# Performance work log

Measured on AMD Instinct MI355X. Metric: run time of the kernel, lower is better.

Reference implementation:

```python
import jax, jax.numpy as jnp
import numpy as np

N = 50000
E = 1600000
B = 64
NODE_DIM = 12
EDGE_DIM = 4
HIDDEN = 128
HEADS = 4
C = HIDDEN // HEADS  # 32
LAYERS = 3
NEG_SLOPE = 0.2
EPS = 1e-16


def _ln(x, g, b):
    m = jnp.mean(x, -1, keepdims=True)
    v = jnp.mean((x - m) ** 2, -1, keepdims=True)
    return (x - m) * jax.lax.rsqrt(v + 1e-5) * g + b


def _gelu(x):
    return jax.nn.gelu(x, approximate=False)


def setup_inputs() -> dict:
    key = jax.random.key(0)
    ks = jax.random.split(key, 20)
    f = lambda k, sh: jax.random.normal(k, sh, jnp.float32) * 0.05
    return {
        "x": jax.random.normal(ks[0], (N, NODE_DIM), jnp.float32),
        "edge_attr": jax.random.normal(ks[1], (E, EDGE_DIM), jnp.float32),
        "edge_index": jax.random.randint(ks[2], (2, E), 0, N, jnp.int32),
        "batch": jnp.sort(jax.random.randint(ks[3], (N,), 0, B, jnp.int32)),
        "enc_w": f(ks[4], (NODE_DIM, HIDDEN)), "enc_b": jnp.zeros(HIDDEN, jnp.float32),
        "enc_g": jnp.ones(HIDDEN, jnp.float32), "enc_beta": jnp.zeros(HIDDEN, jnp.float32),
        "ee_w": f(ks[5], (EDGE_DIM, HIDDEN // 2)), "ee_b": jnp.zeros(HIDDEN // 2, jnp.float32),
        "gat_lin_w": f(ks[6], (LAYERS, HIDDEN, HEADS * C)),
        "gat_edge_w": f(ks[7], (LAYERS, HIDDEN // 2, HEADS * C)),
        "att_src": f(ks[8], (LAYERS, HEADS, C)),
        "att_dst": f(ks[9], (LAYERS, HEADS, C)),
        "att_edge": f(ks[10], (LAYERS, HEADS, C)),
        "gat_bias": jnp.zeros((LAYERS, HEADS * C), jnp.float32),
        "norm_g": jnp.ones((LAYERS, HIDDEN), jnp.float32),
        "norm_b": jnp.zeros((LAYERS, HIDDEN), jnp.float32),
        "freq_w1": f(ks[11], (2 * HIDDEN, HIDDEN)), "freq_b1": jnp.zeros(HIDDEN, jnp.float32),
        "freq_w2": f(ks[12], (HIDDEN, HIDDEN // 2)), "freq_b2": jnp.zeros(HIDDEN // 2, jnp.float32),
        "cls_w1": f(ks[13], (HIDDEN // 2, 64)), "cls_b1": jnp.zeros(64, jnp.float32),
        "cls_w2": f(ks[14], (64, 1)), "cls_b2": jnp.zeros(1, jnp.float32),
    }


def _forward(x, edge_attr, edge_index, batch,
             enc_w, enc_b, enc_g, enc_beta, ee_w, ee_b,
             gat_lin_w, gat_edge_w, att_src, att_dst, att_edge, gat_bias,
             norm_g, norm_b, freq_w1, freq_b1, freq_w2, freq_b2,
             cls_w1, cls_b1, cls_w2, cls_b2):
    n = x.shape[0]
    h = _gelu(_ln(x @ enc_w + enc_b, enc_g, enc_beta))          # [N, HIDDEN]
    ea = _gelu(edge_attr @ ee_w + ee_b)                          # [E, HIDDEN//2]
    src, dst = edge_index[0], edge_index[1]
    # add_self_loops with fill_value='mean': per-dst-node mean of incoming edge attrs
    deg = jax.ops.segment_sum(jnp.ones(src.shape, ea.dtype), dst, n)
    loop_attr = jax.ops.segment_sum(ea, dst, n) / jnp.maximum(deg, 1.0)[:, None]
    ar = jnp.arange(n, dtype=src.dtype)
    s_full = jnp.concatenate([src, ar])
    d_full = jnp.concatenate([dst, ar])
    ea_full = jnp.concatenate([ea, loop_attr], 0)                # [E+N, HIDDEN//2]
    for l in range(LAYERS):
        hh = (h @ gat_lin_w[l]).reshape(n, HEADS, C)             # [N, H, C]
        ef = (ea_full @ gat_edge_w[l]).reshape(-1, HEADS, C)     # [E+N, H, C]
        a_s = jnp.einsum('nhc,hc->nh', hh, att_src[l])
        a_d = jnp.einsum('nhc,hc->nh', hh, att_dst[l])
        alpha = a_s[s_full] + a_d[d_full] + jnp.einsum('ehc,hc->eh', ef, att_edge[l])
        alpha = jnp.where(alpha > 0, alpha, NEG_SLOPE * alpha)   # leaky_relu
        m = jax.ops.segment_max(alpha, d_full, n)                # segment softmax
        ex = jnp.exp(alpha - m[d_full])
        denom = jax.ops.segment_sum(ex, d_full, n)
        w = ex / (denom[d_full] + EPS)                           # [E+N, H]
        agg = jax.ops.segment_sum(w[:, :, None] * hh[s_full], d_full, n)
        agg = agg.reshape(n, HEADS * C) + gat_bias[l]
        h = _ln(h + agg, norm_g[l], norm_b[l])                   # residual + LayerNorm
    cnt = jax.ops.segment_sum(jnp.ones((n,), h.dtype), batch, B)
    mean = jax.ops.segment_sum(h, batch, B) / jnp.maximum(cnt, 1.0)[:, None]
    mx = jax.ops.segment_max(h, batch, B)
    mx = jnp.where(cnt[:, None] > 0, mx, 0.0)
    g = jnp.concatenate([mean, mx], -1)                          # [B, 2*HIDDEN]
    g = _gelu(_gelu(g @ freq_w1 + freq_b1) @ freq_w2 + freq_b2)
    logits = _gelu(g @ cls_w1 + cls_b1) @ cls_w2 + cls_b2
    return jax.nn.sigmoid(logits[:, 0])                          # [B]


def reference(x, edge_attr, edge_index, batch,
              enc_w, enc_b, enc_g, enc_beta, ee_w, ee_b,
              gat_lin_w, gat_edge_w, att_src, att_dst, att_edge, gat_bias,
              norm_g, norm_b, freq_w1, freq_b1, freq_w2, freq_b2,
              cls_w1, cls_b1, cls_w2, cls_b2):
    return _forward(x, edge_attr, edge_index, batch,
                    enc_w, enc_b, enc_g, enc_beta, ee_w, ee_b,
                    gat_lin_w, gat_edge_w, att_src, att_dst, att_edge, gat_bias,
                    norm_g, norm_b, freq_w1, freq_b1, freq_w2, freq_b2,
                    cls_w1, cls_b1, cls_w2, cls_b2)
```

## Files before the change

### kernel.cpp

```cpp
#include <hip/hip_runtime.h>
#include <float.h>
#include <math.h>

#define N_NODES 50000
#define N_EDGES 1600000
#define NB      64
#define HID     128
#define TOT     (N_EDGES + N_NODES)
#define PARTS   16
#define SCAN_NB 196
#define NPART   8
#define PSIZE   6250
#define EPB     1024
#define GM_ROWS 64

typedef __attribute__((ext_vector_type(8))) short short8;
typedef __attribute__((ext_vector_type(4))) float f32x4;
typedef __attribute__((ext_vector_type(2))) float f32x2;

__device__ __forceinline__ float gelu_f(float x){
    return 0.5f * x * (1.0f + erff(x * 0.70710678118654752440f));
}

__device__ __forceinline__ float asf(unsigned int u){
    union { unsigned int i; float f; } c; c.i = u; return c.f;
}
__device__ __forceinline__ float bf2f(unsigned short u){
    return asf(((unsigned int)u) << 16);
}
__device__ __forceinline__ unsigned short f2bf(float x){
    union { float f; unsigned int i; } c; c.f = x;
    unsigned int r = c.i + 0x7fffu + ((c.i >> 16) & 1u);
    return (unsigned short)(r >> 16);
}
__device__ __forceinline__ uint2 pack4(float a, float b, float cc, float d){
    uint2 r;
    r.x = (unsigned int)f2bf(a) | ((unsigned int)f2bf(b) << 16);
    r.y = (unsigned int)f2bf(cc) | ((unsigned int)f2bf(d) << 16);
    return r;
}
__device__ __forceinline__ unsigned short sel_head(uint2 v, int hd){
    return (hd & 2) ? ((hd & 1) ? (unsigned short)(v.y >> 16) : (unsigned short)(v.y & 0xffff))
                    : ((hd & 1) ? (unsigned short)(v.x >> 16) : (unsigned short)(v.x & 0xffff));
}

__device__ __forceinline__ float blk_sum128(float v, float* red){
    #pragma unroll
    for (int m = 32; m > 0; m >>= 1) v += __shfl_xor(v, m, 64);
    __syncthreads();
    if ((threadIdx.x & 63) == 0) red[threadIdx.x >> 6] = v;
    __syncthreads();
    float r = red[0] + red[1];
    __syncthreads();
    return r;
}

__device__ __forceinline__ int blk_scan256(int v, int* wsum){
    int t = threadIdx.x, lane = t & 63, w = t >> 6;
    int x = v;
    #pragma unroll
    for (int off = 1; off < 64; off <<= 1){
        int y = __shfl_up(x, off, 64);
        if (lane >= off) x += y;
    }
    if (lane == 63) wsum[w] = x;
    __syncthreads();
    if (t == 0){
        int s = 0;
        #pragma unroll
        for (int i = 0; i < 4; i++){ int tmp = wsum[i]; wsum[i] = s; s += tmp; }
    }
    __syncthreads();
    return x + wsum[w];
}

__global__ void enc_kernel(const float* __restrict__ x, const float* __restrict__ enc_w,
                           const float* __restrict__ enc_b, const float* __restrict__ enc_g,
                           const float* __restrict__ enc_beta, float* __restrict__ h)
{
    __shared__ float xs[12];
    __shared__ float red[2];
    int n = blockIdx.x, t = threadIdx.x;
    if (t < 12) xs[t] = x[n * 12 + t];
    __syncthreads();
    float acc = enc_b[t];
    #pragma unroll
    for (int k = 0; k < 12; k++) acc += xs[k] * enc_w[k * HID + t];
    float mean = blk_sum128(acc, red) * (1.0f / HID);
    float d = acc - mean;
    float var = blk_sum128(d * d, red) * (1.0f / HID);
    float y = d * rsqrtf(var + 1e-5f) * enc_g[t] + enc_beta[t];
    h[(size_t)n * HID + t] = gelu_f(y);
}

__global__ void count_kernel(const int* __restrict__ ei, int* __restrict__ row_count){
    int part = blockIdx.x & (NPART - 1);
    int slice = blockIdx.x >> 3;
    int lo = part * PSIZE, hi = lo + PSIZE;
    int base = slice * EPB;
    int iend = min(base + EPB, N_EDGES);
    for (int i = base + threadIdx.x; i < iend; i += 256){
        int d = ei[N_EDGES + i];
        if (d >= lo && d < hi) atomicAdd(&row_count[d], 1);
    }
}

__global__ void scan1_kernel(const int* __restrict__ row_count, int* __restrict__ bsum){
    __shared__ int ws[4];
    int i = blockIdx.x * 256 + threadIdx.x;
    int v = (i < N_NODES) ? (row_count[i] + 1) : 0;
    int x = v;
    #pragma unroll
    for (int m = 32; m > 0; m >>= 1) x += __shfl_xor(x, m, 64);
    if ((threadIdx.x & 63) == 0) ws[threadIdx.x >> 6] = x;
    __syncthreads();
    if (threadIdx.x == 0) bsum[blockIdx.x] = ws[0] + ws[1] + ws[2] + ws[3];
}

__global__ void scan2_kernel(int* __restrict__ bsum){
    __shared__ int ws[4];
    int t = threadIdx.x;
    int v = (t < SCAN_NB) ? bsum[t] : 0;
    int incl = blk_scan256(v, ws);
    if (t < SCAN_NB) bsum[t] = incl - v;
}

__global__ void scan3_kernel(const int* __restrict__ row_count, const int* __restrict__ bsum,
                             int* __restrict__ row_ptr, int* __restrict__ cursor){
    __shared__ int ws[4];
    int i = blockIdx.x * 256 + threadIdx.x;
    int v = (i < N_NODES) ? (row_count[i] + 1) : 0;
    int incl = blk_scan256(v, ws) + bsum[blockIdx.x];
    if (i < N_NODES){
        row_ptr[i + 1] = incl;
        cursor[i] = incl - v;
    }
    if (i == 0) row_ptr[0] = 0;
}

__global__ void scatter_kernel(const int* __restrict__ ei, int* __restrict__ cursor,
                               int2* __restrict__ csr_se, int* __restrict__ self_pos,
                               uint2* __restrict__ alp0, uint2* __restrict__ alp1,
                               uint2* __restrict__ alp2){
    int part = blockIdx.x & (NPART - 1);
    int slice = blockIdx.x >> 3;
    int lo = part * PSIZE, hi = lo + PSIZE;
    int base = slice * EPB;
    int iend = min(base + EPB, TOT);
    for (int i = base + threadIdx.x; i < iend; i += 256){
        int d = (i < N_EDGES) ? ei[N_EDGES + i] : (i - N_EDGES);
        if (d < lo || d >= hi) continue;
        int s = (i < N_EDGES) ? ei[i] : d;
        int pos = atomicAdd(&cursor[d], 1);
        csr_se[pos] = make_int2(s, i);
        if (i >= N_EDGES){
            self_pos[d] = pos;
            uint2 z = make_uint2(0u, 0u);
            alp0[pos] = z; alp1[pos] = z; alp2[pos] = z;
        }
    }
}

__global__ void we3_kernel(const float* __restrict__ gat_edge_w, const float* __restrict__ att_edge,
                           float* __restrict__ We3)
{
    int t = threadIdx.x;
    int k = t >> 2, hd = t & 3;
    for (int l = 0; l < 3; l++){
        float s = 0.f;
        #pragma unroll
        for (int c = 0; c < 32; c++)
            s += gat_edge_w[(size_t)l * 64 * HID + k * HID + hd * 32 + c]
               * att_edge[l * HID + hd * 32 + c];
        We3[(l * 64 + k) * 4 + hd] = s;
    }
}

__global__ void ae_pos_kernel(const int2* __restrict__ csr_se, const float4* __restrict__ edge_attr,
                              const float* __restrict__ ee_w, const float* __restrict__ ee_b,
                              const float* __restrict__ We3,
                              uint2* __restrict__ alp0, uint2* __restrict__ alp1,
                              uint2* __restrict__ alp2)
{
    int p = blockIdx.x * 256 + threadIdx.x;
    if (p >= TOT) return;
    int2 se = csr_se[p];
    if (se.y >= N_EDGES) return;
    float4 ea = edge_attr[se.y];
    const f32x2* w0 = (const f32x2*)(ee_w);
    const f32x2* w1 = (const f32x2*)(ee_w + 64);
    const f32x2* w2 = (const f32x2*)(ee_w + 128);
    const f32x2* w3 = (const f32x2*)(ee_w + 192);
    const f32x2* bb = (const f32x2*)(ee_b);
    const f32x2* Wv = (const f32x2*)(We3);

    f32x2 eax = {ea.x, ea.x}, eay = {ea.y, ea.y}, eaz = {ea.z, ea.z}, eaw = {ea.w, ea.w};
    const f32x2 one2 = {1.0f, 1.0f};
    const f32x2 c044 = {0.044715f, 0.044715f};
    const f32x2 kneg = {-2.3021182f, -2.3021182f};

    f32x2 acc[6];
    #pragma unroll
    for (int i = 0; i < 6; i++) acc[i] = (f32x2){0.f, 0.f};

    #pragma unroll 4
    for (int m = 0; m < 32; m++){
        f32x2 u = bb[m];
        u = __builtin_elementwise_fma(eax, w0[m], u);
        u = __builtin_elementwise_fma(eay, w1[m], u);
        u = __builtin_elementwise_fma(eaz, w2[m], u);
        u = __builtin_elementwise_fma(eaw, w3[m], u);
        f32x2 a = u * u;
        f32x2 b = __builtin_elementwise_fma(c044, a, one2);
        f32x2 c = u * kneg;
        f32x2 z = c * b;
        f32x2 e = { exp2f(z.x), exp2f(z.y) };
        f32x2 d = e + one2;
        f32x2 r = { __builtin_amdgcn_rcpf(d.x), __builtin_amdgcn_rcpf(d.y) };
        f32x2 g = u * r;
        f32x2 gx = {g.x, g.x}, gy = {g.y, g.y};
        #pragma unroll
        for (int l = 0; l < 3; l++){
            int base = (l * 64 + 2 * m) * 2;
            acc[l*2+0] = __builtin_elementwise_fma(gx, Wv[base + 0], acc[l*2+0]);
            acc[l*2+1] = __builtin_elementwise_fma(gx, Wv[base + 1], acc[l*2+1]);
            acc[l*2+0] = __builtin_elementwise_fma(gy, Wv[base + 2], acc[l*2+0]);
            acc[l*2+1] = __builtin_elementwise_fma(gy, Wv[base + 3], acc[l*2+1]);
        }
    }
    alp0[p] = pack4(acc[0].x, acc[0].y, acc[1].x, acc[1].y);
    alp1[p] = pack4(acc[2].x, acc[2].y, acc[3].x, acc[3].y);
    alp2[p] = pack4(acc[4].x, acc[4].y, acc[5].x, acc[5].y);
}

__global__ __launch_bounds__(64) void selfae_kernel(
        const int* __restrict__ row_ptr, const int* __restrict__ self_pos,
        uint2* __restrict__ alp0, uint2* __restrict__ alp1, uint2* __restrict__ alp2)
{
    int n = blockIdx.x, t = threadIdx.x;
    int start = row_ptr[n], end = row_ptr[n + 1];
    int sp = self_pos[n];
    float v[12];
    #pragma unroll
    for (int i = 0; i < 12; i++) v[i] = 0.f;
    for (int p = start + t; p < end; p += 64){
        uint2 q0 = alp0[p], q1 = alp1[p], q2 = alp2[p];
        v[0] += asf(q0.x << 16); v[1] += asf(q0.x & 0xffff0000u);
        v[2] += asf(q0.y << 16); v[3] += asf(q0.y & 0xffff0000u);
        v[4] += asf(q1.x << 16); v[5] += asf(q1.x & 0xffff0000u);
        v[6] += asf(q1.y << 16); v[7] += asf(q1.y & 0xffff0000u);
        v[8] += asf(q2.x << 16); v[9] += asf(q2.x & 0xffff0000u);
        v[10] += asf(q2.y << 16); v[11] += asf(q2.y & 0xffff0000u);
    }
    #pragma unroll
    for (int m = 1; m < 64; m <<= 1){
        #pragma unroll
        for (int i = 0; i < 12; i++) v[i] += __shfl_xor(v[i], m, 64);
    }
    if (t == 0){
        float inv = 1.0f / (float)max(end - start - 1, 1);
        alp0[sp] = pack4(v[0]*inv, v[1]*inv, v[2]*inv,  v[3]*inv);
        alp1[sp] = pack4(v[4]*inv, v[5]*inv, v[6]*inv,  v[7]*inv);
        alp2[sp] = pack4(v[8]*inv, v[9]*inv, v[10]*inv, v[11]*inv);
    }
}

__global__ __launch_bounds__(256) void gemm_hh_kernel(
        const float* __restrict__ h, const float* __restrict__ W,
        const float* __restrict__ att_s, const float* __restrict__ att_d,
        unsigned char* __restrict__ hh8, float* __restrict__ a_s,
        float* __restrict__ a_d)
{
    __shared__ __align__(16) unsigned char smem[128 * 136 * 2];
    unsigned short* Wt = (unsigned short*)smem;
    float* Dsh = (float*)smem;
    int t = threadIdx.x;

    for (int i = t; i < 128 * 128; i += 256){
        int k = i >> 7, n = i & 127;
        Wt[n * 136 + k] = f2bf(W[i]);
    }
    __syncthreads();

    int wave = t >> 6, lane = t & 63;
    int mm = lane & 15, quad = lane >> 4;
    int row = blockIdx.x * GM_ROWS + wave * 16 + mm;
    int rclamp = min(row, N_NODES - 1);
    const float* hrow = h + (size_t)rclamp * HID;

    f32x4 acc[8];
    #pragma unroll
    for (int i = 0; i < 8; i++) acc[i] = (f32x4){0.f, 0.f, 0.f, 0.f};

    #pragma unroll
    for (int kc = 0; kc < 4; kc++){
        int k0 = kc * 32 + quad * 8;
        float4 a0 = *(const float4*)(hrow + k0);
        float4 a1 = *(const float4*)(hrow + k0 + 4);
        short8 af;
        af[0] = (short)f2bf(a0.x); af[1] = (short)f2bf(a0.y);
        af[2] = (short)f2bf(a0.z); af[3] = (short)f2bf(a0.w);
        af[4] = (short)f2bf(a1.x); af[5] = (short)f2bf(a1.y);
        af[6] = (short)f2bf(a1.z); af[7] = (short)f2bf(a1.w);
        #pragma unroll
        for (int nt = 0; nt < 8; nt++){
            short8 bf = *(const short8*)&Wt[(nt * 16 + mm) * 136 + k0];
            acc[nt] = __builtin_amdgcn_mfma_f32_16x16x32_bf16(af, bf, acc[nt], 0, 0, 0);
        }
    }
    __syncthreads();

    #pragma unroll
    for (int nt = 0; nt < 8; nt++){
        #pragma unroll
        for (int r = 0; r < 4; r++){
            Dsh[(wave * 16 + quad * 4 + r) * 132 + nt * 16 + mm] = acc[nt][r];
        }
    }
    __syncthreads();

    int c = t & 127, rp = t >> 7;
    float as_w = att_s[c], ad_w = att_d[c];
    int head = c >> 5;
    for (int rr = rp; rr < GM_ROWS; rr += 2){
        int n = blockIdx.x * GM_ROWS + rr;
        if (n >= N_NODES) break;
        float val = Dsh[rr * 132 + c];
        unsigned int pk = (unsigned int)__builtin_amdgcn_cvt_pk_fp8_f32(val, 0.f, 0, false);
        hh8[(size_t)n * HID + c] = (unsigned char)(pk & 0xFFu);
        float vs = val * as_w, vd = val * ad_w;
        #pragma unroll
        for (int m2 = 16; m2 > 0; m2 >>= 1){
            vs += __shfl_xor(vs, m2, 32);
            vd += __shfl_xor(vd, m2, 32);
        }
        if ((c & 31) == 0){
            a_s[n * 4 + head] = vs;
            a_d[n * 4 + head] = vd;
        }
    }
}

__global__ __launch_bounds__(64) void agg_kernel(
        const float* __restrict__ a_s, const float* __restrict__ a_d,
        const int* __restrict__ row_ptr, const int2* __restrict__ csr_se,
        const uint2* __restrict__ alp, const uint2* __restrict__ hhv2,
        float* __restrict__ h, const float* __restrict__ gat_bias,
        const float* __restrict__ norm_g, const float* __restrict__ norm_b)
{
    int n = blockIdx.x, ln = threadIdx.x;
    int g = ln >> 4, l16 = ln & 15, hd = l16 >> 2;
    int start = row_ptr[n], end = row_ptr[n + 1];
    float ad_h = a_d[n * 4 + hd];

    f32x2 a01A = {0.f,0.f}, a23A = {0.f,0.f}, a45A = {0.f,0.f}, a67A = {0.f,0.f};
    f32x2 a01B = {0.f,0.f}, a23B = {0.f,0.f}, a45B = {0.f,0.f}, a67B = {0.f,0.f};
    float exA = 0.f, exB = 0.f;

    auto step = [&](int pp, f32x2& a01, f32x2& a23, f32x2& a45, f32x2& a67, float& es){
        int2 se = csr_se[pp];
        uint2 av = alp[pp];
        float ae = bf2f(sel_head(av, hd));
        float x0 = a_s[se.x * 4 + hd] + ad_h + ae;
        x0 = x0 > 0.f ? x0 : 0.2f * x0;
        float e0 = __expf(x0);
        es += e0;
        uint2 q = hhv2[(size_t)se.x * 16 + l16];
        f32x2 c01 = __builtin_amdgcn_cvt_pk_f32_fp8(q.x, false);
        f32x2 c23 = __builtin_amdgcn_cvt_pk_f32_fp8(q.x, true);
        f32x2 c45 = __builtin_amdgcn_cvt_pk_f32_fp8(q.y, false);
        f32x2 c67 = __builtin_amdgcn_cvt_pk_f32_fp8(q.y, true);
        f32x2 ee = {e0, e0};
        a01 = __builtin_elementwise_fma(ee, c01, a01);
        a23 = __builtin_elementwise_fma(ee, c23, a23);
        a45 = __builtin_elementwise_fma(ee, c45, a45);
        a67 = __builtin_elementwise_fma(ee, c67, a67);
    };

    int p = start + g;
    for (; p + 4 < end; p += 8){
        step(p,     a01A, a23A, a45A, a67A, exA);
        step(p + 4, a01B, a23B, a45B, a67B, exB);
    }
    if (p < end) step(p, a01A, a23A, a45A, a67A, exA);

    f32x2 a01 = a01A + a01B, a23 = a23A + a23B, a45 = a45A + a45B, a67 = a67A + a67B;
    float ex = exA + exB;
    #pragma unroll
    for (int m = 16; m <= 32; m <<= 1){
        a01.x += __shfl_xor(a01.x, m, 64); a01.y += __shfl_xor(a01.y, m, 64);
        a23.x += __shfl_xor(a23.x, m, 64); a23.y += __shfl_xor(a23.y, m, 64);
        a45.x += __shfl_xor(a45.x, m, 64); a45.y += __shfl_xor(a45.y, m, 64);
        a67.x += __shfl_xor(a67.x, m, 64); a67.y += __shfl_xor(a67.y, m, 64);
        ex += __shfl_xor(ex, m, 64);
    }
    float invd = 1.0f / (ex + 1e-16f);

    const float4* hrow4 = (const float4*)(h + (size_t)n * HID);
    float4 hv0 = hrow4[l16 * 2], hv1 = hrow4[l16 * 2 + 1];
    float4 b0 = ((const float4*)gat_bias)[l16 * 2];
    float4 b1 = ((const float4*)gat_bias)[l16 * 2 + 1];
    float y0 = hv0.x + a01.x * invd + b0.x;
    float y1 = hv0.y + a01.y * invd + b0.y;
    float y2 = hv0.z + a23.x * invd + b0.z;
    float y3 = hv0.w + a23.y * invd + b0.w;
    float y4 = hv1.x + a45.x * invd + b1.x;
    float y5 = hv1.y + a45.y * invd + b1.y;
    float y6 = hv1.z + a67.x * invd + b1.z;
    float y7 = hv1.w + a67.y * invd + b1.w;

    float s = y0 + y1 + y2 + y3 + y4 + y5 + y6 + y7;
    #pragma unroll
    for (int m = 1; m <= 8; m <<= 1) s += __shfl_xor(s, m, 64);
    float mean = s * (1.0f / HID);
    float d0 = y0 - mean, d1 = y1 - mean, d2 = y2 - mean, d3 = y3 - mean;
    float d4 = y4 - mean, d5 = y5 - mean, d6 = y6 - mean, d7 = y7 - mean;
    float vsum = d0*d0 + d1*d1 + d2*d2 + d3*d3 + d4*d4 + d5*d5 + d6*d6 + d7*d7;
    #pragma unroll
    for (int m = 1; m <= 8; m <<= 1) vsum += __shfl_xor(vsum, m, 64);
    float rstd = rsqrtf(vsum * (1.0f / HID) + 1e-5f);

    if (ln < 16){
        float4 g0 = ((const float4*)norm_g)[l16 * 2];
        float4 g1 = ((const float4*)norm_g)[l16 * 2 + 1];
        float4 nb0 = ((const float4*)norm_b)[l16 * 2];
        float4 nb1 = ((const float4*)norm_b)[l16 * 2 + 1];
        float4 r0 = make_float4(d0 * rstd * g0.x + nb0.x, d1 * rstd * g0.y + nb0.y,
                                d2 * rstd * g0.z + nb0.z, d3 * rstd * g0.w + nb0.w);
        float4 r1 = make_float4(d4 * rstd * g1.x + nb1.x, d5 * rstd * g1.y + nb1.y,
                                d6 * rstd * g1.z + nb1.z, d7 * rstd * g1.w + nb1.w);
        float4* orow = (float4*)(h + (size_t)n * HID);
        orow[l16 * 2] = r0;
        orow[l16 * 2 + 1] = r1;
    }
}

__global__ void bounds_kernel(const int* __restrict__ batch, int* __restrict__ bstart){
    int b = threadIdx.x;
    if (b > NB) return;
    int lo = 0, hi = N_NODES;
    while (lo < hi){
        int mid = (lo + hi) >> 1;
        if (batch[mid] < b) lo = mid + 1; else hi = mid;
    }
    bstart[b] = lo;
}

__global__ void pool_kernel(const float* __restrict__ h, const int* __restrict__ bstart,
                            float* __restrict__ psum, float* __restrict__ pmax){
    int b = blockIdx.x, part = blockIdx.y, t = threadIdx.x;
    int s = bstart[b], e = bstart[b + 1];
    int len = e - s;
    int chunk = (len + PARTS - 1) / PARTS;
    int cs = s + part * chunk;
    int ce = min(cs + chunk, e);
    float sum = 0.f, mx = -FLT_MAX;
    for (int n = cs; n < ce; ++n){
        float v = h[(size_t)n * HID + t];
        sum += v; mx = fmaxf(mx, v);
    }
    int slot = (b * PARTS + part) * HID + t;
    psum[slot] = sum;
    pmax[slot] = mx;
}

__global__ void mlp_kernel(const float* __restrict__ psum, const float* __restrict__ pmax,
                           const int* __restrict__ bstart,
                           const float* __restrict__ fw1, const float* __restrict__ fb1,
                           const float* __restrict__ fw2, const float* __restrict__ fb2,
                           const float* __restrict__ cw1, const float* __restrict__ cb1,
                           const float* __restrict__ cw2, const float* __restrict__ cb2,
                           float* __restrict__ out)
{
    __shared__ float g[256];
    __shared__ float y1[128];
    __shared__ float y2[64];
    __shared__ float y3[64];
    __shared__ float red[2];
    int b = blockIdx.x, t = threadIdx.x;
    float sum = 0.f, mx = -FLT_MAX;
    for (int p = 0; p < PARTS; p++){
        int slot = (b * PARTS + p) * HID + t;
        sum += psum[slot];
        mx = fmaxf(mx, pmax[slot]);
    }
    int cnt = bstart[b + 1] - bstart[b];
    float mean = sum / (float)max(cnt, 1);
    if (cnt <= 0) mx = 0.f;
    g[t] = mean; g[128 + t] = mx;
    __syncthreads();
    float a1 = fb1[t];
    for (int k = 0; k < 256; k++) a1 += g[k] * fw1[k * 128 + t];
    y1[t] = gelu_f(a1);
    __syncthreads();
    if (t < 64){
        float a2 = fb2[t];
        for (int k = 0; k < 128; k++) a2 += y1[k] * fw2[k * 64 + t];
        y2[t] = gelu_f(a2);
    }
    __syncthreads();
    if (t < 64){
        float a3 = cb1[t];
        for (int k = 0; k < 64; k++) a3 += y2[k] * cw1[k * 64 + t];
        y3[t] = gelu_f(a3);
    }
    __syncthreads();
    float v = (t < 64) ? y3[t] * cw2[t] : 0.f;
    float s = blk_sum128(v, red);
    if (t == 0){
        float logit = s + cb2[0];
        out[b] = 1.0f / (1.0f + expf(-logit));
    }
}

extern "C" void kernel_launch(void* const* d_in, const int* in_sizes, int n_in,
                              void* d_out, int out_size, void* d_ws, size_t ws_size,
                              hipStream_t stream)
{
    const float* x         = (const float*)d_in[0];
    const float* edge_attr = (const float*)d_in[1];
    const int*   edge_idx  = (const int*)  d_in[2];
    const int*   batch     = (const int*)  d_in[3];
    const float* enc_w     = (const float*)d_in[4];
    const float* enc_b     = (const float*)d_in[5];
    const float* enc_g     = (const float*)d_in[6];
    const float* enc_beta  = (const float*)d_in[7];
    const float* ee_w      = (const float*)d_in[8];
    const float* ee_b      = (const float*)d_in[9];
    const float* gat_lin_w = (const float*)d_in[10];
    const float* gat_edge_w= (const float*)d_in[11];
    const float* att_src   = (const float*)d_in[12];
    const float* att_dst   = (const float*)d_in[13];
    const float* att_edge  = (const float*)d_in[14];
    const float* gat_bias  = (const float*)d_in[15];
    const float* norm_g    = (const float*)d_in[16];
    const float* norm_b    = (const float*)d_in[17];
    const float* fw1       = (const float*)d_in[18];
    const float* fb1       = (const float*)d_in[19];
    const float* fw2       = (const float*)d_in[20];
    const float* fb2       = (const float*)d_in[21];
    const float* cw1       = (const float*)d_in[22];
    const float* cb1       = (const float*)d_in[23];
    const float* cw2       = (const float*)d_in[24];
    const float* cb2       = (const float*)d_in[25];
    float* out = (float*)d_out;

    char* wsp = (char*)d_ws;
    size_t off = 0;
    auto alloc = [&](size_t bytes) -> void* {
        void* p = wsp + off;
        off += (bytes + 255) & ~(size_t)255;
        return p;
    };
    float*          h        = (float*)alloc((size_t)N_NODES * HID * 4);
    unsigned char*  hh8      = (unsigned char*)alloc((size_t)N_NODES * HID);
    float*          a_s      = (float*)alloc((size_t)N_NODES * 4 * 4);
    float*          a_d      = (float*)alloc((size_t)N_NODES * 4 * 4);
    uint2*          alp0     = (uint2*)alloc((size_t)TOT * 8);
    uint2*          alp1     = (uint2*)alloc((size_t)TOT * 8);
    uint2*          alp2     = (uint2*)alloc((size_t)TOT * 8);
    int2*           csr_se   = (int2*) alloc((size_t)TOT * 8);
    int*            self_pos = (int*)  alloc((size_t)N_NODES * 4);
    int*            row_ptr  = (int*)  alloc((size_t)(N_NODES + 1) * 4);
    int*            cursor   = (int*)  alloc((size_t)N_NODES * 4);
    int*            row_count= (int*)  alloc((size_t)N_NODES * 4);
    int*            bsum     = (int*)  alloc((size_t)SCAN_NB * 4);
    float*          We3      = (float*)alloc(3 * 64 * 4 * 4);
    int*            bstart   = (int*)  alloc((NB + 1) * 4);
    float*          psum     = (float*)alloc((size_t)NB * PARTS * HID * 4);
    float*          pmax     = (float*)alloc((size_t)NB * PARTS * HID * 4);

    hipLaunchKernelGGL(enc_kernel, dim3(N_NODES), dim3(128), 0, stream,
                       x, enc_w, enc_b, enc_g, enc_beta, h);

    hipMemsetAsync(row_count, 0, (size_t)N_NODES * 4, stream);
    {
        int slices_c = (N_EDGES + EPB - 1) / EPB;
        hipLaunchKernelGGL(count_kernel, dim3(slices_c * NPART), dim3(256), 0, stream,
                           edge_idx, row_count);
    }
    hipLaunchKernelGGL(scan1_kernel, dim3(SCAN_NB), dim3(256), 0, stream, row_count, bsum);
    hipLaunchKernelGGL(scan2_kernel, dim3(1), dim3(256), 0, stream, bsum);
    hipLaunchKernelGGL(scan3_kernel, dim3(SCAN_NB), dim3(256), 0, stream,
                       row_count, bsum, row_ptr, cursor);
    {
        int slices_s = (TOT + EPB - 1) / EPB;
        hipLaunchKernelGGL(scatter_kernel, dim3(slices_s * NPART), dim3(256), 0, stream,
                           edge_idx, cursor, csr_se, self_pos, alp0, alp1, alp2);
    }

    hipLaunchKernelGGL(we3_kernel, dim3(1), dim3(256), 0, stream, gat_edge_w, att_edge, We3);
    hipLaunchKernelGGL(ae_pos_kernel, dim3((TOT + 255) / 256), dim3(256), 0, stream,
                       (const int2*)csr_se, (const float4*)edge_attr, ee_w, ee_b, We3,
                       alp0, alp1, alp2);
    hipLaunchKernelGGL(selfae_kernel, dim3(N_NODES), dim3(64), 0, stream,
                       row_ptr, self_pos, alp0, alp1, alp2);

    uint2* alps[3] = {alp0, alp1, alp2};
    int gemm_blocks = (N_NODES + GM_ROWS - 1) / GM_ROWS;
    for (int l = 0; l < 3; l++){
        hipLaunchKernelGGL(gemm_hh_kernel, dim3(gemm_blocks), dim3(256), 0, stream,
                           h, gat_lin_w + (size_t)l * HID * HID,
                           att_src + (size_t)l * HID, att_dst + (size_t)l * HID,
                           hh8, a_s, a_d);
        hipLaunchKernelGGL(agg_kernel, dim3(N_NODES), dim3(64), 0, stream,
                           a_s, a_d, row_ptr, (const int2*)csr_se,
                           (const uint2*)alps[l], (const uint2*)hh8, h,
                           gat_bias + (size_t)l * HID, norm_g + (size_t)l * HID,
                           norm_b + (size_t)l * HID);
    }

    hipLaunchKernelGGL(bounds_kernel, dim3(1), dim3(128), 0, stream, batch, bstart);
    hipLaunchKernelGGL(pool_kernel, dim3(NB, PARTS), dim3(128), 0, stream, h, bstart, psum, pmax);
    hipLaunchKernelGGL(mlp_kernel, dim3(NB), dim3(128), 0, stream,
                       psum, pmax, bstart, fw1, fb1, fw2, fb2, cw1, cb1, cw2, cb2, out);
}
```

Before: 697.0 us.

## Process 8 edges per wavefront with 16-byte fp8 gathers in aggregation

The aggregation kernel now maps 8 lanes per edge, each loading a uint4 (16 fp8 values), instead of 16 lanes loading a uint2. Each wavefront therefore handles 8 edges concurrently rather than 4, which raises memory-level parallelism on the gathers and halves the per-edge index and attention loads. The cost is more accumulator registers, an extra shuffle stage in the reduction, and wider per-lane epilogue work. Separately, the edge-GELU exp2 call is replaced with the raw hardware exp2 builtin.

```diff
diff --git a/kernel.cpp b/kernel.cpp
--- a/kernel.cpp
+++ b/kernel.cpp
@@ -214,7 +214,7 @@
         f32x2 b = __builtin_elementwise_fma(c044, a, one2);
         f32x2 c = u * kneg;
         f32x2 z = c * b;
-        f32x2 e = { exp2f(z.x), exp2f(z.y) };
+        f32x2 e = { __builtin_amdgcn_exp2f(z.x), __builtin_amdgcn_exp2f(z.y) };
         f32x2 d = e + one2;
         f32x2 r = { __builtin_amdgcn_rcpf(d.x), __builtin_amdgcn_rcpf(d.y) };
         f32x2 g = u * r;
@@ -344,20 +344,21 @@
 __global__ __launch_bounds__(64) void agg_kernel(
         const float* __restrict__ a_s, const float* __restrict__ a_d,
         const int* __restrict__ row_ptr, const int2* __restrict__ csr_se,
-        const uint2* __restrict__ alp, const uint2* __restrict__ hhv2,
+        const uint2* __restrict__ alp, const uint4* __restrict__ hhv4,
         float* __restrict__ h, const float* __restrict__ gat_bias,
         const float* __restrict__ norm_g, const float* __restrict__ norm_b)
 {
     int n = blockIdx.x, ln = threadIdx.x;
-    int g = ln >> 4, l16 = ln & 15, hd = l16 >> 2;
+    int g = ln >> 3, l8 = ln & 7, hd = l8 >> 1;
     int start = row_ptr[n], end = row_ptr[n + 1];
     float ad_h = a_d[n * 4 + hd];
 
-    f32x2 a01A = {0.f,0.f}, a23A = {0.f,0.f}, a45A = {0.f,0.f}, a67A = {0.f,0.f};
-    f32x2 a01B = {0.f,0.f}, a23B = {0.f,0.f}, a45B = {0.f,0.f}, a67B = {0.f,0.f};
+    f32x2 accA[8], accB[8];
+    #pragma unroll
+    for (int i = 0; i < 8; i++){ accA[i] = (f32x2){0.f,0.f}; accB[i] = (f32x2){0.f,0.f}; }
     float exA = 0.f, exB = 0.f;
 
-    auto step = [&](int pp, f32x2& a01, f32x2& a23, f32x2& a45, f32x2& a67, float& es){
+    auto step = [&](int pp, f32x2* acc, float& es){
         int2 se = csr_se[pp];
         uint2 av = alp[pp];
         float ae = bf2f(sel_head(av, hd));
@@ -365,73 +366,82 @@
         x0 = x0 > 0.f ? x0 : 0.2f * x0;
         float e0 = __expf(x0);
         es += e0;
-        uint2 q = hhv2[(size_t)se.x * 16 + l16];
-        f32x2 c01 = __builtin_amdgcn_cvt_pk_f32_fp8(q.x, false);
-        f32x2 c23 = __builtin_amdgcn_cvt_pk_f32_fp8(q.x, true);
-        f32x2 c45 = __builtin_amdgcn_cvt_pk_f32_fp8(q.y, false);
-        f32x2 c67 = __builtin_amdgcn_cvt_pk_f32_fp8(q.y, true);
+        uint4 q = hhv4[(size_t)se.x * 8 + l8];
         f32x2 ee = {e0, e0};
-        a01 = __builtin_elementwise_fma(ee, c01, a01);
-        a23 = __builtin_elementwise_fma(ee, c23, a23);
-        a45 = __builtin_elementwise_fma(ee, c45, a45);
-        a67 = __builtin_elementwise_fma(ee, c67, a67);
+        acc[0] = __builtin_elementwise_fma(ee, __builtin_amdgcn_cvt_pk_f32_fp8(q.x, false), acc[0]);
+        acc[1] = __builtin_elementwise_fma(ee, __builtin_amdgcn_cvt_pk_f32_fp8(q.x, true),  acc[1]);
+        acc[2] = __builtin_elementwise_fma(ee, __builtin_amdgcn_cvt_pk_f32_fp8(q.y, false), acc[2]);
+        acc[3] = __builtin_elementwise_fma(ee, __builtin_amdgcn_cvt_pk_f32_fp8(q.y, true),  acc[3]);
+        acc[4] = __builtin_elementwise_fma(ee, __builtin_amdgcn_cvt_pk_f32_fp8(q.z, false), acc[4]);
+        acc[5] = __builtin_elementwise_fma(ee, __builtin_amdgcn_cvt_pk_f32_fp8(q.z, true),  acc[5]);
+        acc[6] = __builtin_elementwise_fma(ee, __builtin_amdgcn_cvt_pk_f32_fp8(q.w, false), acc[6]);
+        acc[7] = __builtin_elementwise_fma(ee, __builtin_amdgcn_cvt_pk_f32_fp8(q.w, true),  acc[7]);
     };
 
     int p = start + g;
-    for (; p + 4 < end; p += 8){
-        step(p,     a01A, a23A, a45A, a67A, exA);
-        step(p + 4, a01B, a23B, a45B, a67B, exB);
-    }
-    if (p < end) step(p, a01A, a23A, a45A, a67A, exA);
-
-    f32x2 a01 = a01A + a01B, a23 = a23A + a23B, a45 = a45A + a45B, a67 = a67A + a67B;
+    for (; p + 8 < end; p += 16){
+        step(p,     accA, exA);
+        step(p + 8, accB, exB);
+    }
+    if (p < end) step(p, accA, exA);
+
+    f32x2 acc[8];
+    #pragma unroll
+    for (int i = 0; i < 8; i++) acc[i] = accA[i] + accB[i];
     float ex = exA + exB;
     #pragma unroll
-    for (int m = 16; m <= 32; m <<= 1){
-        a01.x += __shfl_xor(a01.x, m, 64); a01.y += __shfl_xor(a01.y, m, 64);
-        a23.x += __shfl_xor(a23.x, m, 64); a23.y += __shfl_xor(a23.y, m, 64);
-        a45.x += __shfl_xor(a45.x, m, 64); a45.y += __shfl_xor(a45.y, m, 64);
-        a67.x += __shfl_xor(a67.x, m, 64); a67.y += __shfl_xor(a67.y, m, 64);
+    for (int m = 8; m <= 32; m <<= 1){
+        #pragma unroll
+        for (int i = 0; i < 8; i++){
+            acc[i].x += __shfl_xor(acc[i].x, m, 64);
+            acc[i].y += __shfl_xor(acc[i].y, m, 64);
+        }
         ex += __shfl_xor(ex, m, 64);
     }
     float invd = 1.0f / (ex + 1e-16f);
 
     const float4* hrow4 = (const float4*)(h + (size_t)n * HID);
-    float4 hv0 = hrow4[l16 * 2], hv1 = hrow4[l16 * 2 + 1];
-    float4 b0 = ((const float4*)gat_bias)[l16 * 2];
-    float4 b1 = ((const float4*)gat_bias)[l16 * 2 + 1];
-    float y0 = hv0.x + a01.x * invd + b0.x;
-    float y1 = hv0.y + a01.y * invd + b0.y;
-    float y2 = hv0.z + a23.x * invd + b0.z;
-    float y3 = hv0.w + a23.y * invd + b0.w;
-    float y4 = hv1.x + a45.x * invd + b1.x;
-    float y5 = hv1.y + a45.y * invd + b1.y;
-    float y6 = hv1.z + a67.x * invd + b1.z;
-    float y7 = hv1.w + a67.y * invd + b1.w;
-
-    float s = y0 + y1 + y2 + y3 + y4 + y5 + y6 + y7;
-    #pragma unroll
-    for (int m = 1; m <= 8; m <<= 1) s += __shfl_xor(s, m, 64);
+    const float4* bias4 = (const float4*)gat_bias;
+    float y[16];
+    #pragma unroll
+    for (int j = 0; j < 4; j++){
+        float4 hv = hrow4[l8 * 4 + j];
+        float4 bv = bias4[l8 * 4 + j];
+        y[j*4+0] = hv.x + acc[j*2+0].x * invd + bv.x;
+        y[j*4+1] = hv.y + acc[j*2+0].y * invd + bv.y;
+        y[j*4+2] = hv.z + acc[j*2+1].x * invd + bv.z;
+        y[j*4+3] = hv.w + acc[j*2+1].y * invd + bv.w;
+    }
+
+    float s = 0.f;
+    #pragma unroll
+    for (int j = 0; j < 16; j++) s += y[j];
+    #pragma unroll
+    for (int m = 1; m <= 4; m <<= 1) s += __shfl_xor(s, m, 64);
     float mean = s * (1.0f / HID);
-    float d0 = y0 - mean, d1 = y1 - mean, d2 = y2 - mean, d3 = y3 - mean;
-    float d4 = y4 - mean, d5 = y5 - mean, d6 = y6 - mean, d7 = y7 - mean;
-    float vsum = d0*d0 + d1*d1 + d2*d2 + d3*d3 + d4*d4 + d5*d5 + d6*d6 + d7*d7;
-    #pragma unroll
-    for (int m = 1; m <= 8; m <<= 1) vsum += __shfl_xor(vsum, m, 64);
+    float d[16];
+    float vsum = 0.f;
+    #pragma unroll
+    for (int j = 0; j < 16; j++){ d[j] = y[j] - mean; vsum += d[j] * d[j]; }
+    #pragma unroll
+    for (int m = 1; m <= 4; m <<= 1) vsum += __shfl_xor(vsum, m, 64);
     float rstd = rsqrtf(vsum * (1.0f / HID) + 1e-5f);
 
-    if (ln < 16){
-        float4 g0 = ((const float4*)norm_g)[l16 * 2];
-        float4 g1 = ((const float4*)norm_g)[l16 * 2 + 1];
-        float4 nb0 = ((const float4*)norm_b)[l16 * 2];
-        float4 nb1 = ((const float4*)norm_b)[l16 * 2 + 1];
-        float4 r0 = make_float4(d0 * rstd * g0.x + nb0.x, d1 * rstd * g0.y + nb0.y,
-                                d2 * rstd * g0.z + nb0.z, d3 * rstd * g0.w + nb0.w);
-        float4 r1 = make_float4(d4 * rstd * g1.x + nb1.x, d5 * rstd * g1.y + nb1.y,
-                                d6 * rstd * g1.z + nb1.z, d7 * rstd * g1.w + nb1.w);
+    if (ln < 8){
+        const float4* g4 = (const float4*)norm_g;
+        const float4* b4 = (const float4*)norm_b;
         float4* orow = (float4*)(h + (size_t)n * HID);
-        orow[l16 * 2] = r0;
-        orow[l16 * 2 + 1] = r1;
+        #pragma unroll
+        for (int j = 0; j < 4; j++){
+            float4 gg = g4[l8 * 4 + j];
+            float4 bb = b4[l8 * 4 + j];
+            float4 r;
+            r.x = d[j*4+0] * rstd * gg.x + bb.x;
+            r.y = d[j*4+1] * rstd * gg.y + bb.y;
+            r.z = d[j*4+2] * rstd * gg.z + bb.z;
+            r.w = d[j*4+3] * rstd * gg.w + bb.w;
+            orow[l8 * 4 + j] = r;
+        }
     }
 }
 
@@ -605,7 +615,7 @@
                            hh8, a_s, a_d);
         hipLaunchKernelGGL(agg_kernel, dim3(N_NODES), dim3(64), 0, stream,
                            a_s, a_d, row_ptr, (const int2*)csr_se,
-                           (const uint2*)alps[l], (const uint2*)hh8, h,
+                           (const uint2*)alps[l], (const uint4*)hh8, h,
                            gat_bias + (size_t)l * HID, norm_g + (size_t)l * HID,
                            norm_b + (size_t)l * HID);
     }
```

After: 717.4 us. 1.03x slower.

## Build CSR with per-edge atomic ranks instead of cursor atomics in scatter

Applied to the files above, without the earlier changes.

The counting pass now records each edge's atomic rank within its destination row, so the scatter pass computes positions as row_ptr plus rank without a second round of atomics. Self-loop entries are placed at the end of each row directly in the scan kernel, which removes the self_pos array. The scatter is re-partitioned into 4 partitions with larger slices. In exchange it adds a 6.4 MB rank buffer to write and read back. Separately, exp2f in the edge-attention kernel is swapped for the hardware exp2 intrinsic.

```diff
diff --git a/kernel.cpp b/kernel.cpp
--- a/kernel.cpp
+++ b/kernel.cpp
@@ -9,9 +9,9 @@
 #define TOT     (N_EDGES + N_NODES)
 #define PARTS   16
 #define SCAN_NB 196
-#define NPART   8
-#define PSIZE   6250
-#define EPB     1024
+#define NPART4  4
+#define PSIZE4  12500
+#define SEPB    2048
 #define GM_ROWS 64
 
 typedef __attribute__((ext_vector_type(8))) short short8;
@@ -93,16 +93,10 @@
     h[(size_t)n * HID + t] = gelu_f(y);
 }
 
-__global__ void count_kernel(const int* __restrict__ ei, int* __restrict__ row_count){
-    int part = blockIdx.x & (NPART - 1);
-    int slice = blockIdx.x >> 3;
-    int lo = part * PSIZE, hi = lo + PSIZE;
-    int base = slice * EPB;
-    int iend = min(base + EPB, N_EDGES);
-    for (int i = base + threadIdx.x; i < iend; i += 256){
-        int d = ei[N_EDGES + i];
-        if (d >= lo && d < hi) atomicAdd(&row_count[d], 1);
-    }
+__global__ void rank_kernel(const int* __restrict__ ei, int* __restrict__ row_count,
+                            int* __restrict__ rank){
+    int i = blockIdx.x * 256 + threadIdx.x;
+    if (i < N_EDGES) rank[i] = atomicAdd(&row_count[ei[N_EDGES + i]], 1);
 }
 
 __global__ void scan1_kernel(const int* __restrict__ row_count, int* __restrict__ bsum){
@@ -126,38 +120,35 @@
 }
 
 __global__ void scan3_kernel(const int* __restrict__ row_count, const int* __restrict__ bsum,
-                             int* __restrict__ row_ptr, int* __restrict__ cursor){
+                             int* __restrict__ row_ptr, int2* __restrict__ csr_se,
+                             uint2* __restrict__ alp0, uint2* __restrict__ alp1,
+                             uint2* __restrict__ alp2){
     __shared__ int ws[4];
     int i = blockIdx.x * 256 + threadIdx.x;
     int v = (i < N_NODES) ? (row_count[i] + 1) : 0;
     int incl = blk_scan256(v, ws) + bsum[blockIdx.x];
     if (i < N_NODES){
         row_ptr[i + 1] = incl;
-        cursor[i] = incl - v;
+        int sp = incl - 1;
+        csr_se[sp] = make_int2(i, N_EDGES);
+        uint2 z = make_uint2(0u, 0u);
+        alp0[sp] = z; alp1[sp] = z; alp2[sp] = z;
     }
     if (i == 0) row_ptr[0] = 0;
 }
 
-__global__ void scatter_kernel(const int* __restrict__ ei, int* __restrict__ cursor,
-                               int2* __restrict__ csr_se, int* __restrict__ self_pos,
-                               uint2* __restrict__ alp0, uint2* __restrict__ alp1,
-                               uint2* __restrict__ alp2){
-    int part = blockIdx.x & (NPART - 1);
-    int slice = blockIdx.x >> 3;
-    int lo = part * PSIZE, hi = lo + PSIZE;
-    int base = slice * EPB;
-    int iend = min(base + EPB, TOT);
+__global__ void scatter_kernel(const int* __restrict__ ei, const int* __restrict__ rank,
+                               const int* __restrict__ row_ptr, int2* __restrict__ csr_se){
+    int part = blockIdx.x & (NPART4 - 1);
+    int slice = blockIdx.x >> 2;
+    int lo = part * PSIZE4, hi = lo + PSIZE4;
+    int base = slice * SEPB;
+    int iend = min(base + SEPB, N_EDGES);
     for (int i = base + threadIdx.x; i < iend; i += 256){
-        int d = (i < N_EDGES) ? ei[N_EDGES + i] : (i - N_EDGES);
+        int d = ei[N_EDGES + i];
         if (d < lo || d >= hi) continue;
-        int s = (i < N_EDGES) ? ei[i] : d;
-        int pos = atomicAdd(&cursor[d], 1);
-        csr_se[pos] = make_int2(s, i);
-        if (i >= N_EDGES){
-            self_pos[d] = pos;
-            uint2 z = make_uint2(0u, 0u);
-            alp0[pos] = z; alp1[pos] = z; alp2[pos] = z;
-        }
+        int pos = row_ptr[d] + rank[i];
+        csr_se[pos] = make_int2(ei[i], i);
     }
 }
 
@@ -214,7 +205,7 @@
         f32x2 b = __builtin_elementwise_fma(c044, a, one2);
         f32x2 c = u * kneg;
         f32x2 z = c * b;
-        f32x2 e = { exp2f(z.x), exp2f(z.y) };
+        f32x2 e = { __builtin_amdgcn_exp2f(z.x), __builtin_amdgcn_exp2f(z.y) };
         f32x2 d = e + one2;
         f32x2 r = { __builtin_amdgcn_rcpf(d.x), __builtin_amdgcn_rcpf(d.y) };
         f32x2 g = u * r;
@@ -234,12 +225,12 @@
 }
 
 __global__ __launch_bounds__(64) void selfae_kernel(
-        const int* __restrict__ row_ptr, const int* __restrict__ self_pos,
+        const int* __restrict__ row_ptr,
         uint2* __restrict__ alp0, uint2* __restrict__ alp1, uint2* __restrict__ alp2)
 {
     int n = blockIdx.x, t = threadIdx.x;
     int start = row_ptr[n], end = row_ptr[n + 1];
-    int sp = self_pos[n];
+    int sp = end - 1;
     float v[12];
     #pragma unroll
     for (int i = 0; i < 12; i++) v[i] = 0.f;
@@ -560,9 +551,8 @@
     uint2*          alp1     = (uint2*)alloc((size_t)TOT * 8);
     uint2*          alp2     = (uint2*)alloc((size_t)TOT * 8);
     int2*           csr_se   = (int2*) alloc((size_t)TOT * 8);
-    int*            self_pos = (int*)  alloc((size_t)N_NODES * 4);
+    int*            rank     = (int*)  alloc((size_t)N_EDGES * 4);
     int*            row_ptr  = (int*)  alloc((size_t)(N_NODES + 1) * 4);
-    int*            cursor   = (int*)  alloc((size_t)N_NODES * 4);
     int*            row_count= (int*)  alloc((size_t)N_NODES * 4);
     int*            bsum     = (int*)  alloc((size_t)SCAN_NB * 4);
     float*          We3      = (float*)alloc(3 * 64 * 4 * 4);
@@ -574,19 +564,16 @@
                        x, enc_w, enc_b, enc_g, enc_beta, h);
 
     hipMemsetAsync(row_count, 0, (size_t)N_NODES * 4, stream);
-    {
-        int slices_c = (N_EDGES + EPB - 1) / EPB;
-        hipLaunchKernelGGL(count_kernel, dim3(slices_c * NPART), dim3(256), 0, stream,
-                           edge_idx, row_count);
-    }
+    hipLaunchKernelGGL(rank_kernel, dim3((N_EDGES + 255) / 256), dim3(256), 0, stream,
+                       edge_idx, row_count, rank);
     hipLaunchKernelGGL(scan1_kernel, dim3(SCAN_NB), dim3(256), 0, stream, row_count, bsum);
     hipLaunchKernelGGL(scan2_kernel, dim3(1), dim3(256), 0, stream, bsum);
     hipLaunchKernelGGL(scan3_kernel, dim3(SCAN_NB), dim3(256), 0, stream,
-                       row_count, bsum, row_ptr, cursor);
+                       row_count, bsum, row_ptr, csr_se, alp0, alp1, alp2);
     {
-        int slices_s = (TOT + EPB - 1) / EPB;
-        hipLaunchKernelGGL(scatter_kernel, dim3(slices_s * NPART), dim3(256), 0, stream,
-                           edge_idx, cursor, csr_se, self_pos, alp0, alp1, alp2);
+        int slices_s = (N_EDGES + SEPB - 1) / SEPB;
+        hipLaunchKernelGGL(scatter_kernel, dim3(slices_s * NPART4), dim3(256), 0, stream,
+                           edge_idx, rank, row_ptr, csr_se);
     }
 
     hipLaunchKernelGGL(we3_kernel, dim3(1), dim3(256), 0, stream, gat_edge_w, att_edge, We3);
@@ -594,7 +581,7 @@
                        (const int2*)csr_se, (const float4*)edge_attr, ee_w, ee_b, We3,
                        alp0, alp1, alp2);
     hipLaunchKernelGGL(selfae_kernel, dim3(N_NODES), dim3(64), 0, stream,
-                       row_ptr, self_pos, alp0, alp1, alp2);
+                       row_ptr, alp0, alp1, alp2);
 
     uint2* alps[3] = {alp0, alp1, alp2};
     int gemm_blocks = (N_NODES + GM_ROWS - 1) / GM_ROWS;
```

New measurement: 641.4 us. 8.0% less time.
